# Kernel optimization log

Hardware: AMD Instinct MI355X
Metric: run time of the kernel (lower is better)

The kernel has to match this reference:

```python
import jax, jax.numpy as jnp
import numpy as np

TEMPERATURE = 0.07
EPS = 1e-8  # torch F.cosine_similarity eps


def _normalize(x):
    # x: [B, D] -> row-normalized with torch-style eps clamp on the norm
    n = jnp.sqrt(jnp.sum(x * x, axis=-1, keepdims=True))
    return x / jnp.maximum(n, EPS)


def setup_inputs() -> dict:
    key = jax.random.key(0)
    k1, k2, k3 = jax.random.split(key, 3)
    B, D, C = 8192, 512, 2048
    return {
        "label_tensor": jax.random.randint(k1, (B,), 0, C, dtype=jnp.int64),
        "feature_a": jax.random.normal(k2, (B, D), dtype=jnp.float32),
        "feature_b": jax.random.normal(k3, (B, D), dtype=jnp.float32),
    }


def reference(label_tensor, feature_a, feature_b):
    # cosine similarity matrix: cos_score[i, j] = cos(a_i, b_j)  -> [B, B]
    a = _normalize(feature_a)
    b = _normalize(feature_b)
    cos_score = jnp.einsum('id,jd->ij', a, b)

    logits = cos_score / TEMPERATURE
    # positives mask: same label (diagonal always True since label[i]==label[i])
    mask = (label_tensor[:, None] == label_tensor[None, :])

    e = jnp.exp(logits)                      # safe: |logits| <= 1/0.07 ~ 14.3
    numerator = jnp.sum(jnp.where(mask, e, 0.0), axis=1)
    denominator = jnp.sum(e, axis=1)
    loss = -jnp.mean(jnp.log(numerator / denominator))
    return loss, cos_score
```

## Files before the change

### kernel.cpp

```cpp
#include <hip/hip_runtime.h>
#include <cstdint>
#include <cstddef>

#define BDIM 8192
#define DDIM 512

typedef __bf16 bf16x8 __attribute__((ext_vector_type(8)));
typedef float f32x4 __attribute__((ext_vector_type(4)));

__device__ inline unsigned short f32_to_bf16(float f) {
    unsigned int u = __float_as_uint(f);
    u += 0x7FFF + ((u >> 16) & 1);
    return (unsigned short)(u >> 16);
}

__global__ __launch_bounds__(256) void normalize_kernel(
    const float* __restrict__ a, const float* __restrict__ b,
    unsigned short* __restrict__ an, unsigned short* __restrict__ bn)
{
    const int lane = threadIdx.x & 63;
    const int row = blockIdx.x * 4 + (threadIdx.x >> 6);
    const float* src;
    unsigned short* dst;
    if (row < BDIM) {
        src = a + (size_t)row * DDIM;
        dst = an + (size_t)row * DDIM;
    } else {
        src = b + (size_t)(row - BDIM) * DDIM;
        dst = bn + (size_t)(row - BDIM) * DDIM;
    }
    const float4* s4 = (const float4*)src;
    float4 v0 = s4[lane];
    float4 v1 = s4[lane + 64];
    float ss = v0.x * v0.x + v0.y * v0.y + v0.z * v0.z + v0.w * v0.w
             + v1.x * v1.x + v1.y * v1.y + v1.z * v1.z + v1.w * v1.w;
#pragma unroll
    for (int m = 1; m < 64; m <<= 1) ss += __shfl_xor(ss, m);
    float inv = 1.0f / fmaxf(sqrtf(ss), 1e-8f);
    ushort4 o0, o1;
    o0.x = f32_to_bf16(v0.x * inv); o0.y = f32_to_bf16(v0.y * inv);
    o0.z = f32_to_bf16(v0.z * inv); o0.w = f32_to_bf16(v0.w * inv);
    o1.x = f32_to_bf16(v1.x * inv); o1.y = f32_to_bf16(v1.y * inv);
    o1.z = f32_to_bf16(v1.z * inv); o1.w = f32_to_bf16(v1.w * inv);
    ushort4* d4 = (ushort4*)dst;
    d4[lane] = o0;
    d4[lane + 64] = o1;
}

__global__ __launch_bounds__(256, 2) void gemm_fused_kernel(
    const unsigned short* __restrict__ an, const unsigned short* __restrict__ bn,
    const int* __restrict__ labels, float* __restrict__ cos_out,
    float* __restrict__ num, float* __restrict__ den)
{
    __shared__ __align__(16) unsigned short sA[128 * 64];
    __shared__ __align__(16) unsigned short sB[256 * 64];

    const int t = threadIdx.x;
    const int wid = t >> 6;
    const int lane = t & 63;
    const int quad = lane >> 4;
    const int lr = lane & 15;
    const int bm = blockIdx.y;
    const int bnb = blockIdx.x;
    const int wm = wid >> 1;
    const int wn = wid & 1;

    f32x4 acc[4][8] = {};

    const char* aBase = (const char*)an;
    const char* bBase = (const char*)bn;
    char* sAB = (char*)sA;
    char* sBB = (char*)sB;

    unsigned gOffA[4], gOffB[8];
#pragma unroll
    for (int c = 0; c < 4; ++c) {
        int li = c * 256 + t;
        int r = li >> 3;
        int cch = (li & 7) ^ (r & 7);
        gOffA[c] = (unsigned)((bm * 128 + r) * (DDIM * 2) + cch * 16);
    }
#pragma unroll
    for (int c = 0; c < 8; ++c) {
        int li = c * 256 + t;
        int r = li >> 3;
        int cch = (li & 7) ^ (r & 7);
        gOffB[c] = (unsigned)((bnb * 256 + r) * (DDIM * 2) + cch * 16);
    }

    for (int k0 = 0; k0 < DDIM; k0 += 64) {
#pragma unroll
        for (int c = 0; c < 4; ++c)
            __builtin_amdgcn_global_load_lds(
                (const __attribute__((address_space(1))) void*)(aBase + gOffA[c] + k0 * 2),
                (__attribute__((address_space(3))) void*)(sAB + c * 4096 + wid * 1024),
                16, 0, 0);
#pragma unroll
        for (int c = 0; c < 8; ++c)
            __builtin_amdgcn_global_load_lds(
                (const __attribute__((address_space(1))) void*)(bBase + gOffB[c] + k0 * 2),
                (__attribute__((address_space(3))) void*)(sBB + c * 4096 + wid * 1024),
                16, 0, 0);
        __syncthreads();
#pragma unroll
        for (int kk = 0; kk < 2; ++kk) {
            bf16x8 af[4], bfr[8];
#pragma unroll
            for (int mi = 0; mi < 4; ++mi) {
                int r = wm * 64 + mi * 16 + lr;
                int cch = (kk * 4 + quad) ^ (r & 7);
                af[mi] = *(const bf16x8*)(sAB + r * 128 + cch * 16);
            }
#pragma unroll
            for (int ni = 0; ni < 8; ++ni) {
                int r = wn * 128 + ni * 16 + lr;
                int cch = (kk * 4 + quad) ^ (r & 7);
                bfr[ni] = *(const bf16x8*)(sBB + r * 128 + cch * 16);
            }
#pragma unroll
            for (int mi = 0; mi < 4; ++mi)
#pragma unroll
                for (int ni = 0; ni < 8; ++ni)
                    acc[mi][ni] = __builtin_amdgcn_mfma_f32_16x16x32_bf16(
                        af[mi], bfr[ni], acc[mi][ni], 0, 0, 0);
        }
        __syncthreads();
    }

    const float INV_T = 1.0f / 0.07f;
    const int col0 = bnb * 256 + wn * 128 + lr;
    int lab_c[8];
#pragma unroll
    for (int ni = 0; ni < 8; ++ni) lab_c[ni] = labels[col0 + ni * 16];

#pragma unroll
    for (int mi = 0; mi < 4; ++mi) {
        int rbase = bm * 128 + wm * 64 + mi * 16 + quad * 4;
#pragma unroll
        for (int r = 0; r < 4; ++r) {
            int row = rbase + r;
            int lab_r = labels[row];
            float dsum = 0.0f, nsum = 0.0f;
#pragma unroll
            for (int ni = 0; ni < 8; ++ni) {
                float cv = acc[mi][ni][r];
                cos_out[(size_t)row * BDIM + col0 + ni * 16] = cv;
                float e = __expf(cv * INV_T);
                dsum += e;
                nsum += (lab_c[ni] == lab_r) ? e : 0.0f;
            }
#pragma unroll
            for (int m = 1; m < 16; m <<= 1) {
                dsum += __shfl_xor(dsum, m);
                nsum += __shfl_xor(nsum, m);
            }
            if (lr == 0) {
                atomicAdd(&den[row], dsum);
                atomicAdd(&num[row], nsum);
            }
        }
    }
}

__global__ __launch_bounds__(1024) void loss_kernel(
    const float* __restrict__ num, const float* __restrict__ den,
    float* __restrict__ out)
{
    int t = threadIdx.x;
    float s = 0.0f;
#pragma unroll
    for (int i = 0; i < 8; ++i) {
        int idx = t + i * 1024;
        s += __logf(num[idx] / den[idx]);
    }
#pragma unroll
    for (int m = 1; m < 64; m <<= 1) s += __shfl_xor(s, m);
    __shared__ float red[16];
    if ((t & 63) == 0) red[t >> 6] = s;
    __syncthreads();
    if (t == 0) {
        float tot = 0.0f;
#pragma unroll
        for (int i = 0; i < 16; ++i) tot += red[i];
        out[0] = -tot / (float)BDIM;
    }
}

extern "C" void kernel_launch(void* const* d_in, const int* in_sizes, int n_in,
                              void* d_out, int out_size, void* d_ws, size_t ws_size,
                              hipStream_t stream)
{
    const int* labels = (const int*)d_in[0];
    const float* fa = (const float*)d_in[1];
    const float* fb = (const float*)d_in[2];
    float* out = (float*)d_out;

    unsigned short* an = (unsigned short*)d_ws;
    unsigned short* bn = an + (size_t)BDIM * DDIM;
    float* num = (float*)(bn + (size_t)BDIM * DDIM);
    float* den = num + BDIM;

    hipMemsetAsync(num, 0, 2 * BDIM * sizeof(float), stream);
    normalize_kernel<<<4096, 256, 0, stream>>>(fa, fb, an, bn);
    dim3 grid(32, 64);
    gemm_fused_kernel<<<grid, 256, 0, stream>>>(an, bn, labels, out + 1, num, den);
    loss_kernel<<<1, 1024, 0, stream>>>(num, den, out);
}
```

Baseline: 395.0 us.

## Use 256x256 tiles with 8 waves and double-buffered pipelined LDS loads

Restructures the fused GEMM to a 256x256 output tile per 512-thread block. The K loop is fully unrolled over a 128KB double-buffered LDS, and global-to-LDS loads are issued in quarter-tile stages interleaved with MFMA quadrants, using explicit vmcnt waits, barriers and setprio. This aims to overlap memory latency with compute and halve global operand traffic per output. The epilogue switches the large cosine matrix writes to nontemporal stores. Occupancy drops to one block per CU because of the large LDS footprint, and the many barriers add sync overhead.

```diff
diff --git a/kernel.cpp b/kernel.cpp
--- a/kernel.cpp
+++ b/kernel.cpp
@@ -47,104 +47,158 @@
     d4[lane + 64] = o1;
 }
 
-__global__ __launch_bounds__(256, 2) void gemm_fused_kernel(
+#define BAR()    __builtin_amdgcn_s_barrier()
+#define WAITV4() asm volatile("s_waitcnt vmcnt(4)" ::: "memory")
+#define WAITV0() asm volatile("s_waitcnt vmcnt(0)" ::: "memory")
+
+__global__ __launch_bounds__(512, 2) void gemm_fused_kernel(
     const unsigned short* __restrict__ an, const unsigned short* __restrict__ bn,
     const int* __restrict__ labels, float* __restrict__ cos_out,
     float* __restrict__ num, float* __restrict__ den)
 {
-    __shared__ __align__(16) unsigned short sA[128 * 64];
-    __shared__ __align__(16) unsigned short sB[256 * 64];
+    __shared__ __align__(16) char lds[131072];
+    char* ldsC = (char*)lds;
 
     const int t = threadIdx.x;
     const int wid = t >> 6;
     const int lane = t & 63;
     const int quad = lane >> 4;
     const int lr = lane & 15;
+    const int sx = lr & 7;
     const int bm = blockIdx.y;
     const int bnb = blockIdx.x;
-    const int wm = wid >> 1;
-    const int wn = wid & 1;
-
-    f32x4 acc[4][8] = {};
-
-    const char* aBase = (const char*)an;
-    const char* bBase = (const char*)bn;
-    char* sAB = (char*)sA;
-    char* sBB = (char*)sB;
-
-    unsigned gOffA[4], gOffB[8];
-#pragma unroll
-    for (int c = 0; c < 4; ++c) {
-        int li = c * 256 + t;
-        int r = li >> 3;
-        int cch = (li & 7) ^ (r & 7);
-        gOffA[c] = (unsigned)((bm * 128 + r) * (DDIM * 2) + cch * 16);
-    }
-#pragma unroll
-    for (int c = 0; c < 8; ++c) {
-        int li = c * 256 + t;
-        int r = li >> 3;
-        int cch = (li & 7) ^ (r & 7);
-        gOffB[c] = (unsigned)((bnb * 256 + r) * (DDIM * 2) + cch * 16);
-    }
-
-    for (int k0 = 0; k0 < DDIM; k0 += 64) {
-#pragma unroll
-        for (int c = 0; c < 4; ++c)
-            __builtin_amdgcn_global_load_lds(
-                (const __attribute__((address_space(1))) void*)(aBase + gOffA[c] + k0 * 2),
-                (__attribute__((address_space(3))) void*)(sAB + c * 4096 + wid * 1024),
-                16, 0, 0);
-#pragma unroll
-        for (int c = 0; c < 8; ++c)
-            __builtin_amdgcn_global_load_lds(
-                (const __attribute__((address_space(1))) void*)(bBase + gOffB[c] + k0 * 2),
-                (__attribute__((address_space(3))) void*)(sBB + c * 4096 + wid * 1024),
-                16, 0, 0);
-        __syncthreads();
-#pragma unroll
-        for (int kk = 0; kk < 2; ++kk) {
-            bf16x8 af[4], bfr[8];
-#pragma unroll
-            for (int mi = 0; mi < 4; ++mi) {
-                int r = wm * 64 + mi * 16 + lr;
-                int cch = (kk * 4 + quad) ^ (r & 7);
-                af[mi] = *(const bf16x8*)(sAB + r * 128 + cch * 16);
-            }
-#pragma unroll
-            for (int ni = 0; ni < 8; ++ni) {
-                int r = wn * 128 + ni * 16 + lr;
-                int cch = (kk * 4 + quad) ^ (r & 7);
-                bfr[ni] = *(const bf16x8*)(sBB + r * 128 + cch * 16);
-            }
+    const int wm = wid >> 2;
+    const int wn = wid & 3;
+
+    f32x4 acc[8][4] = {};
+
+    unsigned rowOff[2], ldsW[2];
+#pragma unroll
+    for (int j = 0; j < 2; ++j) {
+        int li = (j * 8 + wid) * 64 + lane;
+        int r  = li >> 3;
+        int gc = (li & 7) ^ (r & 7);
+        rowOff[j] = (unsigned)(r * (DDIM * 2) + gc * 16);
+        ldsW[j]   = (unsigned)((j * 8 + wid) * 1024);
+    }
+    const char* aT = (const char*)an + (size_t)(bm * 256) * (DDIM * 2);
+    const char* bT = (const char*)bn + (size_t)(bnb * 256) * (DDIM * 2);
+
+    auto STG = [&](int i) {
+        const int tile = i >> 2, role = i & 3;
+        const int isA = (role == 1 || role == 2);
+        const int h   = (role == 2 || role == 3);
+        const unsigned ldsBase = (unsigned)((tile & 1) * 65536) +
+                                 (isA ? 0u : 32768u) + (unsigned)(h * 16384);
+        const char* g = (isA ? aT : bT) + h * (128 * DDIM * 2) + tile * 128;
+        __builtin_amdgcn_global_load_lds(
+            (const __attribute__((address_space(1))) void*)(g + rowOff[0]),
+            (__attribute__((address_space(3))) void*)(ldsC + ldsBase + ldsW[0]), 16, 0, 0);
+        __builtin_amdgcn_global_load_lds(
+            (const __attribute__((address_space(1))) void*)(g + rowOff[1]),
+            (__attribute__((address_space(3))) void*)(ldsC + ldsBase + ldsW[1]), 16, 0, 0);
+    };
+
+    bf16x8 afA[4][2], afB[4][2], bfA[2][2], bfB[2][2];
+
+    auto MMAQ = [&](int mh, int nh, bf16x8 (&afX)[4][2], bf16x8 (&bfX)[2][2]) {
+        __builtin_amdgcn_s_setprio(1);
+#pragma unroll
+        for (int kk = 0; kk < 2; ++kk)
 #pragma unroll
             for (int mi = 0; mi < 4; ++mi)
 #pragma unroll
-                for (int ni = 0; ni < 8; ++ni)
-                    acc[mi][ni] = __builtin_amdgcn_mfma_f32_16x16x32_bf16(
-                        af[mi], bfr[ni], acc[mi][ni], 0, 0, 0);
-        }
-        __syncthreads();
+                for (int ni = 0; ni < 2; ++ni)
+                    acc[mh * 4 + mi][nh * 2 + ni] =
+                        __builtin_amdgcn_mfma_f32_16x16x32_bf16(
+                            afX[mi][kk], bfX[ni][kk],
+                            acc[mh * 4 + mi][nh * 2 + ni], 0, 0, 0);
+        __builtin_amdgcn_s_setprio(0);
+    };
+
+    STG(0); STG(1); STG(2); STG(3); STG(4); STG(5);
+    WAITV4();
+    BAR();
+
+#pragma unroll
+    for (int T = 0; T < 8; ++T) {
+        const unsigned bufO  = (unsigned)((T & 1) * 65536);
+        const unsigned aBase = bufO + (unsigned)(wm * 16384);
+        const unsigned bBase = bufO + 32768u + (unsigned)((wn >> 1) * 16384);
+        const int brp = (wn & 1) * 64;
+
+#pragma unroll
+        for (int mi = 0; mi < 4; ++mi)
+#pragma unroll
+            for (int kk = 0; kk < 2; ++kk) {
+                int rp = mi * 16 + lr;
+                afA[mi][kk] = *(const bf16x8*)(ldsC + aBase + rp * 128 +
+                                               (((kk * 4 + quad) ^ sx) << 4));
+            }
+#pragma unroll
+        for (int ni = 0; ni < 2; ++ni)
+#pragma unroll
+            for (int kk = 0; kk < 2; ++kk) {
+                int rp = brp + ni * 16 + lr;
+                bfA[ni][kk] = *(const bf16x8*)(ldsC + bBase + rp * 128 +
+                                               (((kk * 4 + quad) ^ sx) << 4));
+            }
+        if (6 + 4 * T < 32) STG(6 + 4 * T);
+        BAR();
+        MMAQ(0, 0, afA, bfA);
+        BAR();
+
+#pragma unroll
+        for (int ni = 0; ni < 2; ++ni)
+#pragma unroll
+            for (int kk = 0; kk < 2; ++kk) {
+                int rp = brp + (ni + 2) * 16 + lr;
+                bfB[ni][kk] = *(const bf16x8*)(ldsC + bBase + rp * 128 +
+                                               (((kk * 4 + quad) ^ sx) << 4));
+            }
+        if (7 + 4 * T < 32) STG(7 + 4 * T);
+        BAR();
+        MMAQ(0, 1, afA, bfB);
+        BAR();
+
+#pragma unroll
+        for (int mi = 0; mi < 4; ++mi)
+#pragma unroll
+            for (int kk = 0; kk < 2; ++kk) {
+                int rp = (mi + 4) * 16 + lr;
+                afB[mi][kk] = *(const bf16x8*)(ldsC + aBase + rp * 128 +
+                                               (((kk * 4 + quad) ^ sx) << 4));
+            }
+        if (8 + 4 * T < 32) STG(8 + 4 * T);
+        BAR();
+        MMAQ(1, 1, afB, bfB);
+        BAR();
+
+        if (9 + 4 * T < 32) STG(9 + 4 * T);
+        BAR();
+        MMAQ(1, 0, afB, bfA);
+        if (T < 6) { WAITV4(); BAR(); }
+        else if (T == 6) { WAITV0(); BAR(); }
     }
 
     const float INV_T = 1.0f / 0.07f;
-    const int col0 = bnb * 256 + wn * 128 + lr;
-    int lab_c[8];
-#pragma unroll
-    for (int ni = 0; ni < 8; ++ni) lab_c[ni] = labels[col0 + ni * 16];
-
-#pragma unroll
-    for (int mi = 0; mi < 4; ++mi) {
-        int rbase = bm * 128 + wm * 64 + mi * 16 + quad * 4;
+    const int col0 = bnb * 256 + wn * 64 + lr;
+    int lab_c[4];
+#pragma unroll
+    for (int ni = 0; ni < 4; ++ni) lab_c[ni] = labels[col0 + ni * 16];
+
+#pragma unroll
+    for (int mi = 0; mi < 8; ++mi) {
+        int rbase = bm * 256 + wm * 128 + mi * 16 + quad * 4;
 #pragma unroll
         for (int r = 0; r < 4; ++r) {
             int row = rbase + r;
             int lab_r = labels[row];
             float dsum = 0.0f, nsum = 0.0f;
 #pragma unroll
-            for (int ni = 0; ni < 8; ++ni) {
+            for (int ni = 0; ni < 4; ++ni) {
                 float cv = acc[mi][ni][r];
-                cos_out[(size_t)row * BDIM + col0 + ni * 16] = cv;
+                __builtin_nontemporal_store(cv, &cos_out[(size_t)row * BDIM + col0 + ni * 16]);
                 float e = __expf(cv * INV_T);
                 dsum += e;
                 nsum += (lab_c[ni] == lab_r) ? e : 0.0f;
@@ -202,7 +256,7 @@
 
     hipMemsetAsync(num, 0, 2 * BDIM * sizeof(float), stream);
     normalize_kernel<<<4096, 256, 0, stream>>>(fa, fb, an, bn);
-    dim3 grid(32, 64);
-    gemm_fused_kernel<<<grid, 256, 0, stream>>>(an, bn, labels, out + 1, num, den);
+    dim3 grid(32, 32);
+    gemm_fused_kernel<<<grid, 512, 0, stream>>>(an, bn, labels, out + 1, num, den);
     loss_kernel<<<1, 1024, 0, stream>>>(num, den, out);
 }
```

Result: slower. 417.5 us (+5.7%).

## Shrink GEMM tile, stage output through LDS for coalesced nontemporal stores

Applied to the files above, without the earlier changes.

Reduces the block tile from 128x256 to 128x128 so fewer accumulators are live and three blocks can share a CU, and doubles the grid to match. The epilogue transposes each 16x64 accumulator patch through LDS so every lane writes a contiguous float4 to the 256 MB cos_score output with nontemporal stores, replacing scattered 4-byte stores. Per-row num/den partials from the two column warps are combined in LDS before issuing one atomic per row, which halves atomic traffic. The cost is more redundant A-tile loads from global memory and extra LDS round trips and barriers in the epilogue.

```diff
diff --git a/kernel.cpp b/kernel.cpp
--- a/kernel.cpp
+++ b/kernel.cpp
@@ -47,13 +47,15 @@
     d4[lane + 64] = o1;
 }
 
-__global__ __launch_bounds__(256, 2) void gemm_fused_kernel(
+__global__ __launch_bounds__(256, 3) void gemm_fused_kernel(
     const unsigned short* __restrict__ an, const unsigned short* __restrict__ bn,
     const int* __restrict__ labels, float* __restrict__ cos_out,
     float* __restrict__ num, float* __restrict__ den)
 {
-    __shared__ __align__(16) unsigned short sA[128 * 64];
-    __shared__ __align__(16) unsigned short sB[256 * 64];
+    __shared__ __align__(16) char lds[32768];
+    char* ldsC = (char*)lds;
+    char* sA = ldsC;
+    char* sB = ldsC + 16384;
 
     const int t = threadIdx.x;
     const int wid = t >> 6;
@@ -65,87 +67,88 @@
     const int wm = wid >> 1;
     const int wn = wid & 1;
 
-    f32x4 acc[4][8] = {};
-
-    const char* aBase = (const char*)an;
-    const char* bBase = (const char*)bn;
-    char* sAB = (char*)sA;
-    char* sBB = (char*)sB;
-
-    unsigned gOffA[4], gOffB[8];
+    f32x4 acc[4][4] = {};
+
+    unsigned gOffA[4], gOffB[4];
 #pragma unroll
     for (int c = 0; c < 4; ++c) {
         int li = c * 256 + t;
         int r = li >> 3;
         int cch = (li & 7) ^ (r & 7);
         gOffA[c] = (unsigned)((bm * 128 + r) * (DDIM * 2) + cch * 16);
-    }
-#pragma unroll
-    for (int c = 0; c < 8; ++c) {
-        int li = c * 256 + t;
-        int r = li >> 3;
-        int cch = (li & 7) ^ (r & 7);
-        gOffB[c] = (unsigned)((bnb * 256 + r) * (DDIM * 2) + cch * 16);
-    }
+        gOffB[c] = (unsigned)((bnb * 128 + r) * (DDIM * 2) + cch * 16);
+    }
+    const char* aBase = (const char*)an;
+    const char* bBase = (const char*)bn;
 
     for (int k0 = 0; k0 < DDIM; k0 += 64) {
 #pragma unroll
         for (int c = 0; c < 4; ++c)
             __builtin_amdgcn_global_load_lds(
                 (const __attribute__((address_space(1))) void*)(aBase + gOffA[c] + k0 * 2),
-                (__attribute__((address_space(3))) void*)(sAB + c * 4096 + wid * 1024),
+                (__attribute__((address_space(3))) void*)(sA + c * 4096 + t * 16),
                 16, 0, 0);
 #pragma unroll
-        for (int c = 0; c < 8; ++c)
+        for (int c = 0; c < 4; ++c)
             __builtin_amdgcn_global_load_lds(
                 (const __attribute__((address_space(1))) void*)(bBase + gOffB[c] + k0 * 2),
-                (__attribute__((address_space(3))) void*)(sBB + c * 4096 + wid * 1024),
+                (__attribute__((address_space(3))) void*)(sB + c * 4096 + t * 16),
                 16, 0, 0);
         __syncthreads();
-#pragma unroll
-        for (int kk = 0; kk < 2; ++kk) {
-            bf16x8 af[4], bfr[8];
-#pragma unroll
-            for (int mi = 0; mi < 4; ++mi) {
-                int r = wm * 64 + mi * 16 + lr;
-                int cch = (kk * 4 + quad) ^ (r & 7);
-                af[mi] = *(const bf16x8*)(sAB + r * 128 + cch * 16);
-            }
-#pragma unroll
-            for (int ni = 0; ni < 8; ++ni) {
-                int r = wn * 128 + ni * 16 + lr;
-                int cch = (kk * 4 + quad) ^ (r & 7);
-                bfr[ni] = *(const bf16x8*)(sBB + r * 128 + cch * 16);
-            }
+
+        bf16x8 af[4][2], bf[4][2];
+#pragma unroll
+        for (int mi = 0; mi < 4; ++mi)
+#pragma unroll
+            for (int kk = 0; kk < 2; ++kk) {
+                int rp = wm * 64 + mi * 16 + lr;
+                af[mi][kk] = *(const bf16x8*)(sA + rp * 128 +
+                                              (((kk * 4 + quad) ^ (rp & 7)) << 4));
+            }
+#pragma unroll
+        for (int ni = 0; ni < 4; ++ni)
+#pragma unroll
+            for (int kk = 0; kk < 2; ++kk) {
+                int rp = wn * 64 + ni * 16 + lr;
+                bf[ni][kk] = *(const bf16x8*)(sB + rp * 128 +
+                                              (((kk * 4 + quad) ^ (rp & 7)) << 4));
+            }
+#pragma unroll
+        for (int kk = 0; kk < 2; ++kk)
 #pragma unroll
             for (int mi = 0; mi < 4; ++mi)
 #pragma unroll
-                for (int ni = 0; ni < 8; ++ni)
+                for (int ni = 0; ni < 4; ++ni)
                     acc[mi][ni] = __builtin_amdgcn_mfma_f32_16x16x32_bf16(
-                        af[mi], bfr[ni], acc[mi][ni], 0, 0, 0);
-        }
+                        af[mi][kk], bf[ni][kk], acc[mi][ni], 0, 0, 0);
         __syncthreads();
     }
 
     const float INV_T = 1.0f / 0.07f;
-    const int col0 = bnb * 256 + wn * 128 + lr;
-    int lab_c[8];
-#pragma unroll
-    for (int ni = 0; ni < 8; ++ni) lab_c[ni] = labels[col0 + ni * 16];
+    const int col0 = bnb * 128 + wn * 64 + lr;
+    int lab_c[4];
+#pragma unroll
+    for (int ni = 0; ni < 4; ++ni) lab_c[ni] = labels[col0 + ni * 16];
+
+    float* patch = (float*)(ldsC + wid * 4352);
+    float* part  = (float*)(ldsC + 17408);
 
 #pragma unroll
     for (int mi = 0; mi < 4; ++mi) {
-        int rbase = bm * 128 + wm * 64 + mi * 16 + quad * 4;
+#pragma unroll
+        for (int ni = 0; ni < 4; ++ni)
+#pragma unroll
+            for (int r = 0; r < 4; ++r)
+                patch[(quad * 4 + r) * 68 + ni * 16 + lr] = acc[mi][ni][r];
+
 #pragma unroll
         for (int r = 0; r < 4; ++r) {
-            int row = rbase + r;
-            int lab_r = labels[row];
+            int rowL = wm * 64 + mi * 16 + quad * 4 + r;
+            int lab_r = labels[bm * 128 + rowL];
             float dsum = 0.0f, nsum = 0.0f;
 #pragma unroll
-            for (int ni = 0; ni < 8; ++ni) {
-                float cv = acc[mi][ni][r];
-                cos_out[(size_t)row * BDIM + col0 + ni * 16] = cv;
-                float e = __expf(cv * INV_T);
+            for (int ni = 0; ni < 4; ++ni) {
+                float e = __expf(acc[mi][ni][r] * INV_T);
                 dsum += e;
                 nsum += (lab_c[ni] == lab_r) ? e : 0.0f;
             }
@@ -155,10 +158,27 @@
                 nsum += __shfl_xor(nsum, m);
             }
             if (lr == 0) {
-                atomicAdd(&den[row], dsum);
-                atomicAdd(&num[row], nsum);
+                float2 pv; pv.x = nsum; pv.y = dsum;
+                *(float2*)&part[(size_t)(wn * 128 + rowL) * 2] = pv;
             }
         }
+
+#pragma unroll
+        for (int p = 0; p < 4; ++p) {
+            f32x4 v = *(const f32x4*)&patch[(p * 4 + quad) * 68 + lr * 4];
+            int row = bm * 128 + wm * 64 + mi * 16 + p * 4 + quad;
+            f32x4* gp = (f32x4*)&cos_out[(size_t)row * BDIM + bnb * 128 + wn * 64 + lr * 4];
+            __builtin_nontemporal_store(v, gp);
+        }
+    }
+
+    __syncthreads();
+    if (t < 128) {
+        float2 p0 = *(float2*)&part[(size_t)(0 * 128 + t) * 2];
+        float2 p1 = *(float2*)&part[(size_t)(1 * 128 + t) * 2];
+        int row = bm * 128 + t;
+        atomicAdd(&num[row], p0.x + p1.x);
+        atomicAdd(&den[row], p0.y + p1.y);
     }
 }
 
@@ -202,7 +222,7 @@
 
     hipMemsetAsync(num, 0, 2 * BDIM * sizeof(float), stream);
     normalize_kernel<<<4096, 256, 0, stream>>>(fa, fb, an, bn);
-    dim3 grid(32, 64);
+    dim3 grid(64, 64);
     gemm_fused_kernel<<<grid, 256, 0, stream>>>(an, bn, labels, out + 1, num, den);
     loss_kernel<<<1, 1024, 0, stream>>>(num, den, out);
 }
```

Result: faster. 369.8 us (-6.4%).
